# Kernel tuning notes

Measured on AMD Instinct MI355X. Metric: run time of the kernel, lower is better.

## Reference

```python
import jax, jax.numpy as jnp
import numpy as np

T, B, F, L = 512, 4096, 16, 4  # seq_len, batch, input_size, n_layers; hidden_size H = 1


def _lstm_layer(seq, W_ih, W_hh, b_ih, b_hh):
    """Single unidirectional LSTM layer, H=1.
    seq: [T, B, in]; W_ih: [4, in]; W_hh: [4, 1]; b_ih, b_hh: [4].
    Returns (hs [T,B,1], h_T [B,1], c_T [B,1]). Gate order i,f,g,o (PyTorch).
    """
    # Input contribution for all timesteps at once (the only sizeable GEMM).
    gx = jnp.einsum('tbi,gi->tbg', seq, W_ih) + b_ih + b_hh  # [T, B, 4]
    Bb = seq.shape[1]
    h0 = jnp.zeros((Bb, 1), seq.dtype)
    c0 = jnp.zeros((Bb, 1), seq.dtype)

    def step(carry, g):
        h, c = carry
        gates = g + h @ W_hh.T  # [B, 4]
        i = jax.nn.sigmoid(gates[:, 0:1])
        f = jax.nn.sigmoid(gates[:, 1:2])
        gg = jnp.tanh(gates[:, 2:3])
        o = jax.nn.sigmoid(gates[:, 3:4])
        c = f * c + i * gg
        h = o * jnp.tanh(c)
        return (h, c), h

    (hT, cT), hs = jax.lax.scan(step, (h0, c0), gx)
    return hs, hT, cT


def setup_inputs() -> dict:
    key = jax.random.key(0)
    ks = jax.random.split(key, 6)
    s = 0.5  # ~U(-1,1) stdev scale; 1/sqrt(H)=1 in torch init
    return {
        'x': jax.random.normal(ks[0], (T, B, F), jnp.float32),
        'W_ih0': jax.random.normal(ks[1], (4, F), jnp.float32) * s,
        'W_ih_rest': jax.random.normal(ks[2], (L - 1, 4, 1), jnp.float32) * s,
        'W_hh': jax.random.normal(ks[3], (L, 4, 1), jnp.float32) * s,
        'b_ih': jax.random.normal(ks[4], (L, 4), jnp.float32) * s,
        'b_hh': jax.random.normal(ks[5], (L, 4), jnp.float32) * s,
    }


def reference(x, W_ih0, W_ih_rest, W_hh, b_ih, b_hh):
    seq = x
    hns, cns = [], []
    for l in range(L):
        W_ih_l = W_ih0 if l == 0 else W_ih_rest[l - 1]
        seq, hT, cT = _lstm_layer(seq, W_ih_l, W_hh[l], b_ih[l], b_hh[l])
        hns.append(hT)
        cns.append(cT)
    output = seq                      # [T, B, 1] last-layer hidden sequence
    hn = jnp.stack(hns, axis=0)       # [L, B, 1]
    cn = jnp.stack(cns, axis=0)       # [L, B, 1]
    return output, hn, cn
```

## Files before the change

kernel.cpp:

```cpp
#include <hip/hip_runtime.h>

#define T_DIM 512
#define B_DIM 4096
#define L_DIM 4
#define LOG2E 1.44269504088896f

typedef float f4 __attribute__((ext_vector_type(4)));

template <int CTRL>
__device__ __forceinline__ float dpp_mov(float v) {
  int r = __builtin_amdgcn_update_dpp(0, __builtin_bit_cast(int, v), CTRL, 0xf, 0xf, true);
  return __builtin_bit_cast(float, r);
}
template <int CTRL>
__device__ __forceinline__ float qp_add(float v) { return v + dpp_mov<CTRL>(v); }

__device__ __forceinline__ void ld_f4(f4& dst, unsigned voff, const f4* base) {
  asm volatile("global_load_dwordx4 %0, %1, %2"
               : "=v"(dst) : "v"(voff), "s"(base) : "memory");
}
__device__ __forceinline__ void wait8(f4& a0, f4& a1, f4& a2, f4& a3,
                                      f4& a4, f4& a5, f4& a6, f4& a7) {
  asm volatile("s_waitcnt vmcnt(0)"
               : "+v"(a0), "+v"(a1), "+v"(a2), "+v"(a3),
                 "+v"(a4), "+v"(a5), "+v"(a6), "+v"(a7) :: "memory");
}

__global__ __launch_bounds__(64, 1) void lstm_fused(
    const float* __restrict__ x,
    const float* __restrict__ Wih0,
    const float* __restrict__ Wrest,
    const float* __restrict__ Whh,
    const float* __restrict__ bih, const float* __restrict__ bhh,
    float* __restrict__ out) {
  const int lane = threadIdx.x;
  const int g = lane & 3;
  const int l = (lane >> 2) & 3;
  const int c = (lane >> 4) & 3;
  const int chain = blockIdx.x * 4 + c;
  const bool l0 = (l == 0);

  auto sg = [](int i) { return (i == 2) ? 2.0f * LOG2E : -LOG2E; };

  const float whh  = sg(g) * Whh[l * 4 + g];
  const float wih  = l0 ? 0.f : sg(g) * Wrest[(l - 1) * 4 + g];
  const float base = l0 ? 0.f : sg(g) * (bih[l * 4 + g] + bhh[l * 4 + g]);
  f4 wx;
  {
    const f4 wv = ((const f4*)Wih0)[g * 4 + l];
    const float s = sg(g);
    wx.x = s * wv.x; wx.y = s * wv.y; wx.z = s * wv.z; wx.w = s * wv.w;
  }
  const float dinit = l0 ? sg(g) * (bih[g] + bhh[g]) : 0.f;
  const float vm = (g == 2) ? -2.f : 1.f;
  const float va = (g == 2) ? 1.f : 0.f;

  float* __restrict__ po = out + chain;
  float h = 0.f, cs = 0.f;
  float hs0, hs1, hs2, hs3, hs4, hs5, hs6, hs7;

  const char* xb = (const char*)x + (size_t)blockIdx.x * 256;
  const unsigned voff = (unsigned)(c * 64 + l * 16);

  f4 A0, A1, A2, A3, A4, A5, A6, A7;
  f4 B0, B1, B2, B3, B4, B5, B6, B7;

#define LOAD8(R, t0)                                                        \
  do {                                                                      \
    const f4* _p = (const f4*)(xb + (size_t)(t0) * 262144);                 \
    ld_f4(R##0, voff + 0u * 262144u, _p);                                   \
    ld_f4(R##1, voff + 1u * 262144u, _p);                                   \
    ld_f4(R##2, voff + 2u * 262144u, _p);                                   \
    ld_f4(R##3, voff + 3u * 262144u, _p);                                   \
    ld_f4(R##4, voff + 4u * 262144u, _p);                                   \
    ld_f4(R##5, voff + 5u * 262144u, _p);                                   \
    ld_f4(R##6, voff + 6u * 262144u, _p);                                   \
    ld_f4(R##7, voff + 7u * 262144u, _p);                                   \
  } while (0)

#define WAITR(R) wait8(R##0, R##1, R##2, R##3, R##4, R##5, R##6, R##7)

  auto dotD = [&](f4 xv) -> float {
    float p = fmaf(xv.x, wx.x, fmaf(xv.y, wx.y, fmaf(xv.z, wx.z, fmaf(xv.w, wx.w, dinit))));
    p = qp_add<0x124>(p);
    p = qp_add<0x128>(p);
    return p;
  };

  auto cellv = [&](int k, float D, bool guard) -> float {
    float hin = dpp_mov<0x114>(h);
    float pb = l0 ? D : base;
    float gate = fmaf(whh, h, fmaf(wih, hin, pb));

    float r = __builtin_amdgcn_rcpf(1.0f + __builtin_amdgcn_exp2f(gate));
    float v = fmaf(vm, r, va);

    float i_ = dpp_mov<0x00>(v);
    float f_ = dpp_mov<0x55>(v);
    float tg = dpp_mov<0xAA>(v);
    float o_ = dpp_mov<0xFF>(v);
    float cn = fmaf(f_, cs, i_ * tg);
    float tcn = fmaf(-2.0f,
        __builtin_amdgcn_rcpf(1.0f + __builtin_amdgcn_exp2f(2.88539008178f * cn)), 1.0f);
    float hm = o_ * tcn;

    if (guard) {
      const int t = k - l;
      const bool valid = (unsigned)t < (unsigned)T_DIM;
      cs = valid ? cn : cs;
      h  = valid ? hm : h;
    } else {
      cs = cn; h = hm;
    }
    return hm;
  };

#define CELLS8(R, k0, guard)                                                \
  do {                                                                      \
    float D0_ = dotD(R##0), D1_ = dotD(R##1), D2_ = dotD(R##2),             \
          D3_ = dotD(R##3), D4_ = dotD(R##4), D5_ = dotD(R##5),             \
          D6_ = dotD(R##6), D7_ = dotD(R##7);                               \
    hs0 = cellv((k0) + 0, D0_, guard);                                      \
    hs1 = cellv((k0) + 1, D1_, guard);                                      \
    hs2 = cellv((k0) + 2, D2_, guard);                                      \
    hs3 = cellv((k0) + 3, D3_, guard);                                      \
    hs4 = cellv((k0) + 4, D4_, guard);                                      \
    hs5 = cellv((k0) + 5, D5_, guard);                                      \
    hs6 = cellv((k0) + 6, D6_, guard);                                      \
    hs7 = cellv((k0) + 7, D7_, guard);                                      \
  } while (0)

#define FLUSH(k0, jlo, jhi)                                                 \
  do {                                                                      \
    if (l == 3 && g == 0) {                                                 \
      if (0 >= (jlo) && 0 <= (jhi)) po[(size_t)((k0) + 0 - 3) * B_DIM] = hs0; \
      if (1 >= (jlo) && 1 <= (jhi)) po[(size_t)((k0) + 1 - 3) * B_DIM] = hs1; \
      if (2 >= (jlo) && 2 <= (jhi)) po[(size_t)((k0) + 2 - 3) * B_DIM] = hs2; \
      if (3 >= (jlo) && 3 <= (jhi)) po[(size_t)((k0) + 3 - 3) * B_DIM] = hs3; \
      if (4 >= (jlo) && 4 <= (jhi)) po[(size_t)((k0) + 4 - 3) * B_DIM] = hs4; \
      if (5 >= (jlo) && 5 <= (jhi)) po[(size_t)((k0) + 5 - 3) * B_DIM] = hs5; \
      if (6 >= (jlo) && 6 <= (jhi)) po[(size_t)((k0) + 6 - 3) * B_DIM] = hs6; \
      if (7 >= (jlo) && 7 <= (jhi)) po[(size_t)((k0) + 7 - 3) * B_DIM] = hs7; \
    }                                                                       \
  } while (0)

  LOAD8(A, 0);
  WAITR(A);
  LOAD8(B, 8);
  CELLS8(A, 0, true);
  WAITR(B); FLUSH(0, 3, 7);  LOAD8(A, 16);  CELLS8(B, 8, false);
  WAITR(A); FLUSH(8, 0, 7);  LOAD8(B, 24);  CELLS8(A, 16, false);
#pragma unroll 1
  for (int n = 3; n < 63; n += 2) {
    WAITR(B); FLUSH(8 * (n - 1), 0, 7); LOAD8(A, 8 * (n + 1));
    CELLS8(B, 8 * n, false);
    WAITR(A); FLUSH(8 * n, 0, 7);       LOAD8(B, 8 * (n + 2));
    CELLS8(A, 8 * (n + 1), false);
  }
  WAITR(B); FLUSH(8 * 62, 0, 7);
  CELLS8(B, 504, false);
  FLUSH(504, 0, 7);
  CELLS8(B, 512, true);
  FLUSH(512, 0, 2);

  if (g == 0) {
    po[(size_t)T_DIM * B_DIM + (size_t)l * B_DIM] = h;
    po[(size_t)T_DIM * B_DIM + (size_t)L_DIM * B_DIM + (size_t)l * B_DIM] = cs;
  }
#undef LOAD8
#undef WAITR
#undef CELLS8
#undef FLUSH
}

extern "C" void kernel_launch(void* const* d_in, const int* in_sizes, int n_in,
                              void* d_out, int out_size, void* d_ws, size_t ws_size,
                              hipStream_t stream) {
  const float* x     = (const float*)d_in[0];
  const float* Wih0  = (const float*)d_in[1];
  const float* Wrest = (const float*)d_in[2];
  const float* Whh   = (const float*)d_in[3];
  const float* bih   = (const float*)d_in[4];
  const float* bhh   = (const float*)d_in[5];
  float* out = (float*)d_out;
  lstm_fused<<<B_DIM / 4, 64, 0, stream>>>(x, Wih0, Wrest, Whh, bih, bhh, out);
}
```

Baseline: 238.2 us.

## Replace inline-asm loads with plain loads, pack four waves per block, store inline

```diff
diff --git a/kernel.cpp b/kernel.cpp
--- a/kernel.cpp
+++ b/kernel.cpp
@@ -15,29 +15,20 @@
 template <int CTRL>
 __device__ __forceinline__ float qp_add(float v) { return v + dpp_mov<CTRL>(v); }
 
-__device__ __forceinline__ void ld_f4(f4& dst, unsigned voff, const f4* base) {
-  asm volatile("global_load_dwordx4 %0, %1, %2"
-               : "=v"(dst) : "v"(voff), "s"(base) : "memory");
-}
-__device__ __forceinline__ void wait8(f4& a0, f4& a1, f4& a2, f4& a3,
-                                      f4& a4, f4& a5, f4& a6, f4& a7) {
-  asm volatile("s_waitcnt vmcnt(0)"
-               : "+v"(a0), "+v"(a1), "+v"(a2), "+v"(a3),
-                 "+v"(a4), "+v"(a5), "+v"(a6), "+v"(a7) :: "memory");
-}
-
-__global__ __launch_bounds__(64, 1) void lstm_fused(
+__global__ __launch_bounds__(256, 1) void lstm_fused(
     const float* __restrict__ x,
     const float* __restrict__ Wih0,
     const float* __restrict__ Wrest,
     const float* __restrict__ Whh,
     const float* __restrict__ bih, const float* __restrict__ bhh,
     float* __restrict__ out) {
-  const int lane = threadIdx.x;
+  const int tid = threadIdx.x;
+  const int lane = tid & 63;
+  const int wid = tid >> 6;
   const int g = lane & 3;
   const int l = (lane >> 2) & 3;
   const int c = (lane >> 4) & 3;
-  const int chain = blockIdx.x * 4 + c;
+  const int chain = blockIdx.x * 16 + wid * 4 + c;
   const bool l0 = (l == 0);
 
   auto sg = [](int i) { return (i == 2) ? 2.0f * LOG2E : -LOG2E; };
@@ -55,30 +46,24 @@
   const float vm = (g == 2) ? -2.f : 1.f;
   const float va = (g == 2) ? 1.f : 0.f;
 
+  const f4* __restrict__ xp = (const f4*)x;
+  const size_t xoff = (size_t)chain * 4 + (size_t)l;
   float* __restrict__ po = out + chain;
+
   float h = 0.f, cs = 0.f;
-  float hs0, hs1, hs2, hs3, hs4, hs5, hs6, hs7;
-
-  const char* xb = (const char*)x + (size_t)blockIdx.x * 256;
-  const unsigned voff = (unsigned)(c * 64 + l * 16);
-
-  f4 A0, A1, A2, A3, A4, A5, A6, A7;
-  f4 B0, B1, B2, B3, B4, B5, B6, B7;
+  f4 A[8], B[8];
 
 #define LOAD8(R, t0)                                                        \
   do {                                                                      \
-    const f4* _p = (const f4*)(xb + (size_t)(t0) * 262144);                 \
-    ld_f4(R##0, voff + 0u * 262144u, _p);                                   \
-    ld_f4(R##1, voff + 1u * 262144u, _p);                                   \
-    ld_f4(R##2, voff + 2u * 262144u, _p);                                   \
-    ld_f4(R##3, voff + 3u * 262144u, _p);                                   \
-    ld_f4(R##4, voff + 4u * 262144u, _p);                                   \
-    ld_f4(R##5, voff + 5u * 262144u, _p);                                   \
-    ld_f4(R##6, voff + 6u * 262144u, _p);                                   \
-    ld_f4(R##7, voff + 7u * 262144u, _p);                                   \
+    R[0] = xp[(size_t)((t0) + 0) * 16384 + xoff];                           \
+    R[1] = xp[(size_t)((t0) + 1) * 16384 + xoff];                           \
+    R[2] = xp[(size_t)((t0) + 2) * 16384 + xoff];                           \
+    R[3] = xp[(size_t)((t0) + 3) * 16384 + xoff];                           \
+    R[4] = xp[(size_t)((t0) + 4) * 16384 + xoff];                           \
+    R[5] = xp[(size_t)((t0) + 5) * 16384 + xoff];                           \
+    R[6] = xp[(size_t)((t0) + 6) * 16384 + xoff];                           \
+    R[7] = xp[(size_t)((t0) + 7) * 16384 + xoff];                           \
   } while (0)
-
-#define WAITR(R) wait8(R##0, R##1, R##2, R##3, R##4, R##5, R##6, R##7)
 
   auto dotD = [&](f4 xv) -> float {
     float p = fmaf(xv.x, wx.x, fmaf(xv.y, wx.y, fmaf(xv.z, wx.z, fmaf(xv.w, wx.w, dinit))));
@@ -87,7 +72,7 @@
     return p;
   };
 
-  auto cellv = [&](int k, float D, bool guard) -> float {
+  auto cellv = [&](int k, float D, bool guard) {
     float hin = dpp_mov<0x114>(h);
     float pb = l0 ? D : base;
     float gate = fmaf(whh, h, fmaf(wih, hin, pb));
@@ -105,72 +90,51 @@
     float hm = o_ * tcn;
 
     if (guard) {
-      const int t = k - l;
-      const bool valid = (unsigned)t < (unsigned)T_DIM;
+      const bool valid = (unsigned)(k - l) < (unsigned)T_DIM;
       cs = valid ? cn : cs;
       h  = valid ? hm : h;
     } else {
       cs = cn; h = hm;
     }
-    return hm;
+    const int t = k - 3;
+    if (l == 3 && g == 0 && (unsigned)t < (unsigned)T_DIM)
+      po[(size_t)t * B_DIM] = hm;
   };
 
 #define CELLS8(R, k0, guard)                                                \
   do {                                                                      \
-    float D0_ = dotD(R##0), D1_ = dotD(R##1), D2_ = dotD(R##2),             \
-          D3_ = dotD(R##3), D4_ = dotD(R##4), D5_ = dotD(R##5),             \
-          D6_ = dotD(R##6), D7_ = dotD(R##7);                               \
-    hs0 = cellv((k0) + 0, D0_, guard);                                      \
-    hs1 = cellv((k0) + 1, D1_, guard);                                      \
-    hs2 = cellv((k0) + 2, D2_, guard);                                      \
-    hs3 = cellv((k0) + 3, D3_, guard);                                      \
-    hs4 = cellv((k0) + 4, D4_, guard);                                      \
-    hs5 = cellv((k0) + 5, D5_, guard);                                      \
-    hs6 = cellv((k0) + 6, D6_, guard);                                      \
-    hs7 = cellv((k0) + 7, D7_, guard);                                      \
-  } while (0)
-
-#define FLUSH(k0, jlo, jhi)                                                 \
-  do {                                                                      \
-    if (l == 3 && g == 0) {                                                 \
-      if (0 >= (jlo) && 0 <= (jhi)) po[(size_t)((k0) + 0 - 3) * B_DIM] = hs0; \
-      if (1 >= (jlo) && 1 <= (jhi)) po[(size_t)((k0) + 1 - 3) * B_DIM] = hs1; \
-      if (2 >= (jlo) && 2 <= (jhi)) po[(size_t)((k0) + 2 - 3) * B_DIM] = hs2; \
-      if (3 >= (jlo) && 3 <= (jhi)) po[(size_t)((k0) + 3 - 3) * B_DIM] = hs3; \
-      if (4 >= (jlo) && 4 <= (jhi)) po[(size_t)((k0) + 4 - 3) * B_DIM] = hs4; \
-      if (5 >= (jlo) && 5 <= (jhi)) po[(size_t)((k0) + 5 - 3) * B_DIM] = hs5; \
-      if (6 >= (jlo) && 6 <= (jhi)) po[(size_t)((k0) + 6 - 3) * B_DIM] = hs6; \
-      if (7 >= (jlo) && 7 <= (jhi)) po[(size_t)((k0) + 7 - 3) * B_DIM] = hs7; \
-    }                                                                       \
+    float D0_ = dotD(R[0]), D1_ = dotD(R[1]), D2_ = dotD(R[2]),             \
+          D3_ = dotD(R[3]), D4_ = dotD(R[4]), D5_ = dotD(R[5]),             \
+          D6_ = dotD(R[6]), D7_ = dotD(R[7]);                               \
+    cellv((k0) + 0, D0_, guard);                                            \
+    cellv((k0) + 1, D1_, guard);                                            \
+    cellv((k0) + 2, D2_, guard);                                            \
+    cellv((k0) + 3, D3_, guard);                                            \
+    cellv((k0) + 4, D4_, guard);                                            \
+    cellv((k0) + 5, D5_, guard);                                            \
+    cellv((k0) + 6, D6_, guard);                                            \
+    cellv((k0) + 7, D7_, guard);                                            \
   } while (0)
 
   LOAD8(A, 0);
-  WAITR(A);
   LOAD8(B, 8);
   CELLS8(A, 0, true);
-  WAITR(B); FLUSH(0, 3, 7);  LOAD8(A, 16);  CELLS8(B, 8, false);
-  WAITR(A); FLUSH(8, 0, 7);  LOAD8(B, 24);  CELLS8(A, 16, false);
 #pragma unroll 1
-  for (int n = 3; n < 63; n += 2) {
-    WAITR(B); FLUSH(8 * (n - 1), 0, 7); LOAD8(A, 8 * (n + 1));
+  for (int n = 1; n < 63; n += 2) {
+    LOAD8(A, 8 * (n + 1));
     CELLS8(B, 8 * n, false);
-    WAITR(A); FLUSH(8 * n, 0, 7);       LOAD8(B, 8 * (n + 2));
+    LOAD8(B, 8 * (n + 2));
     CELLS8(A, 8 * (n + 1), false);
   }
-  WAITR(B); FLUSH(8 * 62, 0, 7);
   CELLS8(B, 504, false);
-  FLUSH(504, 0, 7);
   CELLS8(B, 512, true);
-  FLUSH(512, 0, 2);
 
   if (g == 0) {
     po[(size_t)T_DIM * B_DIM + (size_t)l * B_DIM] = h;
     po[(size_t)T_DIM * B_DIM + (size_t)L_DIM * B_DIM + (size_t)l * B_DIM] = cs;
   }
 #undef LOAD8
-#undef WAITR
 #undef CELLS8
-#undef FLUSH
 }
 
 extern "C" void kernel_launch(void* const* d_in, const int* in_sizes, int n_in,
@@ -183,5 +147,5 @@
   const float* bih   = (const float*)d_in[4];
   const float* bhh   = (const float*)d_in[5];
   float* out = (float*)d_out;
-  lstm_fused<<<B_DIM / 4, 64, 0, stream>>>(x, Wih0, Wrest, Whh, bih, bhh, out);
+  lstm_fused<<<B_DIM / 16, 256, 0, stream>>>(x, Wih0, Wrest, Whh, bih, bhh, out);
 }
```

After: 219.8 us. -7.7%, faster.
